# Optimization experiments

Hardware: AMD Instinct MI355X
Metric: run time of the kernel (lower is better)

Reference implementation:

```python
import jax, jax.numpy as jnp
import numpy as np

MAX_K = 4
KAPPA_MAX = 80.0
TEMP = 0.7

NPOINT1, NSAMPLE1 = 128, 32
NPOINT2, NSAMPLE2 = 32, 32


def _sqdist(a, b):
    # a: (B,M,3), b: (B,N,3) -> (B,M,N) squared euclidean distance
    return (jnp.sum(a * a, -1)[:, :, None] + jnp.sum(b * b, -1)[:, None, :]
            - 2.0 * jnp.einsum('bmc,bnc->bmn', a, b))


def _fps(xyz, npoint):
    # farthest point sampling, sequential over npoint (inherent recurrence)
    B, N, _ = xyz.shape
    def step(carry, _):
        dist, far = carry
        centroid = jnp.take_along_axis(xyz, far[:, None, None], axis=1)  # (B,1,3)
        d = jnp.sum((xyz - centroid) ** 2, -1)                            # (B,N)
        dist = jnp.minimum(dist, d)
        nxt = jnp.argmax(dist, -1).astype(jnp.int32)
        return (dist, nxt), far
    init = (jnp.full((B, N), 1e10, xyz.dtype), jnp.zeros((B,), jnp.int32))
    _, idx = jax.lax.scan(step, init, None, length=npoint)
    return jnp.transpose(idx)  # (B, npoint)


def _gather(x, idx):
    # x: (B,N,C), idx: (B,...) int -> (B,...,C)
    return jax.vmap(lambda xb, ib: xb[ib])(x, idx)


def _sa(xyz, feats, npoint, nsample, params, group_all=False):
    # PointNet++ set abstraction: FPS + kNN grouping + shared MLP + max-pool
    if group_all:
        new_xyz = jnp.zeros((xyz.shape[0], 1, 3), xyz.dtype)
        g = xyz[:, None]                                   # (B,1,N,3)
        if feats is not None:
            g = jnp.concatenate([g, feats[:, None]], -1)   # (B,1,N,3+C)
    else:
        fidx = _fps(xyz, npoint)                           # (B,S)
        new_xyz = _gather(xyz, fidx)                       # (B,S,3)
        d = _sqdist(new_xyz, xyz)                          # (B,S,N)
        _, nidx = jax.lax.top_k(-d, nsample)               # (B,S,K) nearest
        g = _gather(xyz, nidx) - new_xyz[:, :, None]       # relative coords
        if feats is not None:
            g = jnp.concatenate([g, _gather(feats, nidx)], -1)
    for w, b in params:                                    # shared 1x1 MLP
        g = jax.nn.relu(g @ w + b)
    return new_xyz, jnp.max(g, axis=2)                     # max over group


def _ln(x, g, b, eps=1e-5):
    m = jnp.mean(x, -1, keepdims=True)
    v = jnp.var(x, -1, keepdims=True)
    return (x - m) * jax.lax.rsqrt(v + eps) * g + b


def setup_inputs() -> dict:
    key = jax.random.key(0)
    ks = iter(jax.random.split(key, 64))
    def p(shape, s=0.05):
        return jax.random.normal(next(ks), shape, jnp.float32) * s
    d = {"xyz": jax.random.normal(next(ks), (32, 16384, 3), jnp.float32)}
    sa_dims = {"sa1": [3, 64, 64, 128], "sa2": [131, 128, 128, 256], "sa3": [259, 256, 512, 1024]}
    for name, dims in sa_dims.items():
        for i in range(3):
            d[f"{name}_w{i}"] = p((dims[i], dims[i + 1]))
            d[f"{name}_b{i}"] = jnp.zeros((dims[i + 1],), jnp.float32)
    d["fc1_w"] = p((1024, 512)); d["fc1_b"] = jnp.zeros((512,), jnp.float32)
    d["ln1_g"] = jnp.ones((512,), jnp.float32); d["ln1_b"] = jnp.zeros((512,), jnp.float32)
    d["fc2_w"] = p((512, 256)); d["fc2_b"] = jnp.zeros((256,), jnp.float32)
    d["ln2_g"] = jnp.ones((256,), jnp.float32); d["ln2_b"] = jnp.zeros((256,), jnp.float32)
    d["pi_w"] = p((256, MAX_K)); d["pi_b"] = jnp.zeros((MAX_K,), jnp.float32)
    d["mu_w"] = p((256, MAX_K * 2)); d["mu_b"] = jnp.zeros((MAX_K * 2,), jnp.float32)
    d["kappa_w"] = p((256, MAX_K)); d["kappa_b"] = jnp.zeros((MAX_K,), jnp.float32)
    return d


def reference(xyz,
              sa1_w0, sa1_b0, sa1_w1, sa1_b1, sa1_w2, sa1_b2,
              sa2_w0, sa2_b0, sa2_w1, sa2_b1, sa2_w2, sa2_b2,
              sa3_w0, sa3_b0, sa3_w1, sa3_b1, sa3_w2, sa3_b2,
              fc1_w, fc1_b, ln1_g, ln1_b, fc2_w, fc2_b, ln2_g, ln2_b,
              pi_w, pi_b, mu_w, mu_b, kappa_w, kappa_b):
    l1x, l1f = _sa(xyz, None, NPOINT1, NSAMPLE1,
                   [(sa1_w0, sa1_b0), (sa1_w1, sa1_b1), (sa1_w2, sa1_b2)])
    l2x, l2f = _sa(l1x, l1f, NPOINT2, NSAMPLE2,
                   [(sa2_w0, sa2_b0), (sa2_w1, sa2_b1), (sa2_w2, sa2_b2)])
    _, l3f = _sa(l2x, l2f, None, None,
                 [(sa3_w0, sa3_b0), (sa3_w1, sa3_b1), (sa3_w2, sa3_b2)], group_all=True)
    x = l3f.reshape(l3f.shape[0], -1)  # (B,1024)
    x = jax.nn.relu(_ln(x @ fc1_w + fc1_b, ln1_g, ln1_b))  # dropout is identity in eval
    x = jax.nn.relu(_ln(x @ fc2_w + fc2_b, ln2_g, ln2_b))
    weight = jax.nn.softmax((x @ pi_w + pi_b) / TEMP, axis=-1)
    mu_raw = (x @ mu_w + mu_b).reshape(-1, MAX_K, 2)
    nrm = jnp.linalg.norm(mu_raw, axis=-1, keepdims=True)
    mu_unit = mu_raw / jnp.maximum(nrm, 1e-4)              # F.normalize(eps=1e-4)
    c, s = mu_unit[..., 0], mu_unit[..., 1]
    n2 = jnp.sqrt(c * c + s * s)
    mask = n2 < 1e-3
    c = jnp.where(mask, 1.0, c)
    s = jnp.where(mask, 0.0, s)
    mu = jnp.arctan2(s, c)
    kappa = jnp.minimum(jax.nn.softplus(x @ kappa_w + kappa_b) + 1e-6, KAPPA_MAX)
    return mu, kappa, weight
```

## Files before the change

kernel.cpp:

```cpp
#include <hip/hip_runtime.h>
#include <math.h>

#define B 32
#define N1 16384
#define NP1 128
#define NS1 32
#define NP2 32
#define NS2 32

#define OFF_L1X   0
#define OFF_G1    12288
#define OFF_L1F   405504
#define OFF_L2X   929792
#define OFF_NIDX2 932864
#define OFF_L2F   965632
#define OFF_L3F   1227776

__global__ __launch_bounds__(1024) void k_fps1(const float* __restrict__ xyz,
                                               float* __restrict__ l1x) {
  const int b = blockIdx.x, t = threadIdx.x;
  const float* xb = xyz + (size_t)b * N1 * 3;
  float px[16], py[16], pz[16], dd[16];
#pragma unroll
  for (int j = 0; j < 16; ++j) {
    int idx = t + (j << 10);
    px[j] = xb[idx * 3 + 0]; py[j] = xb[idx * 3 + 1]; pz[j] = xb[idx * 3 + 2];
    dd[j] = 1e10f;
  }
  __shared__ float swv[16]; __shared__ int swi[16];
  __shared__ float s_cx, s_cy, s_cz; __shared__ int s_far;
  if (t == 0) { s_cx = xb[0]; s_cy = xb[1]; s_cz = xb[2]; }
  __syncthreads();
  for (int it = 0; it < NP1; ++it) {
    float cx = s_cx, cy = s_cy, cz = s_cz;
    if (t == 0) {
      float* o = l1x + ((size_t)b * NP1 + it) * 3;
      o[0] = cx; o[1] = cy; o[2] = cz;
    }
    float bd = -1.f; int bi = 0x7fffffff;
#pragma unroll
    for (int j = 0; j < 16; ++j) {
      float dx = px[j] - cx, dy = py[j] - cy, dz = pz[j] - cz;
      float d = dx * dx + dy * dy + dz * dz;
      float nd = fminf(dd[j], d);
      dd[j] = nd;
      if (nd > bd) { bd = nd; bi = t + (j << 10); }
    }
#pragma unroll
    for (int off = 32; off > 0; off >>= 1) {
      float od = __shfl_down(bd, off);
      int oi = __shfl_down(bi, off);
      if (od > bd || (od == bd && oi < bi)) { bd = od; bi = oi; }
    }
    if ((t & 63) == 0) { swv[t >> 6] = bd; swi[t >> 6] = bi; }
    __syncthreads();
    if (t < 64) {
      if (t < 16) { bd = swv[t]; bi = swi[t]; } else { bd = -1.f; bi = 0x7fffffff; }
#pragma unroll
      for (int off = 8; off > 0; off >>= 1) {
        float od = __shfl_down(bd, off);
        int oi = __shfl_down(bi, off);
        if (od > bd || (od == bd && oi < bi)) { bd = od; bi = oi; }
      }
      if (t == 0) s_far = bi;
    }
    __syncthreads();
    int far = s_far;
    if (t == (far & 1023)) {
      int jw = far >> 10;
#pragma unroll
      for (int j = 0; j < 16; ++j)
        if (j == jw) { s_cx = px[j]; s_cy = py[j]; s_cz = pz[j]; }
    }
    __syncthreads();
  }
}

__device__ __forceinline__ float dist3(const float* __restrict__ xb, int idx,
                                       float cx, float cy, float cz,
                                       float& x, float& y, float& z) {
  x = xb[idx * 3 + 0]; y = xb[idx * 3 + 1]; z = xb[idx * 3 + 2];
  float dx = x - cx, dy = y - cy, dz = z - cz;
  return dx * dx + dy * dy + dz * dz;
}

#define KNN_CAP 512
#define NBIN 2048

__global__ __launch_bounds__(256) void k_knn1(const float* __restrict__ xyz,
                                              const float* __restrict__ l1x,
                                              float* __restrict__ g1) {
  const int t = threadIdx.x;
  const int b = blockIdx.x & 31;
  const int m = blockIdx.x >> 5;
  const float* xb = xyz + (size_t)b * N1 * 3;
  const float* cp = l1x + ((size_t)b * NP1 + m) * 3;
  const float cx = cp[0], cy = cp[1], cz = cp[2];

  __shared__ int hist[NBIN];
  __shared__ float cd[KNN_CAP]; __shared__ int ci[KNN_CAP];
  __shared__ float cpx[KNN_CAP], cpy[KNN_CAP], cpz[KNN_CAP];
  __shared__ int s_cnt, s_cut;
  __shared__ int wsum[4];

  for (int i = t; i < NBIN; i += 256) hist[i] = 0;
  if (t == 0) { s_cnt = 0; s_cut = NBIN - 1; }
  __syncthreads();

  for (int j = 0; j < 64; ++j) {
    float x, y, z;
    float d = dist3(xb, t + (j << 8), cx, cy, cz, x, y, z);
    atomicAdd(&hist[__float_as_uint(d) >> 20], 1);
  }
  __syncthreads();

  {
    int loc = 0;
#pragma unroll
    for (int j = 0; j < 8; ++j) loc += hist[t * 8 + j];
    int v = loc;
#pragma unroll
    for (int off = 1; off < 64; off <<= 1) {
      int u = __shfl_up(v, off);
      if ((t & 63) >= off) v += u;
    }
    if ((t & 63) == 63) wsum[t >> 6] = v;
    __syncthreads();
    int woff = 0;
    for (int w = 0; w < (t >> 6); ++w) woff += wsum[w];
    int incl = v + woff, excl = incl - loc;
    if (excl < NS1 && incl >= NS1) {
      int c = excl;
#pragma unroll
      for (int j = 0; j < 8; ++j) {
        c += hist[t * 8 + j];
        if (c >= NS1) { s_cut = t * 8 + j; break; }
      }
    }
  }
  __syncthreads();
  const unsigned cut = (unsigned)s_cut + 1u;

  for (int j = 0; j < 64; ++j) {
    float x, y, z;
    float d = dist3(xb, t + (j << 8), cx, cy, cz, x, y, z);
    if ((__float_as_uint(d) >> 20) <= cut) {
      int p = atomicAdd(&s_cnt, 1);
      if (p < KNN_CAP) { cd[p] = d; ci[p] = t + (j << 8); cpx[p] = x; cpy[p] = y; cpz[p] = z; }
    }
  }
  __syncthreads();
  const int cnt = (s_cnt < KNN_CAP) ? s_cnt : KNN_CAP;

  float* gout = g1 + ((size_t)(b * NP1 + m)) * NS1 * 3;
  for (int p = t; p < cnt; p += 256) {
    const float dp = cd[p]; const int ip = ci[p];
    int rank = 0;
    for (int q = 0; q < cnt; ++q) {
      float dq = cd[q];
      rank += (dq < dp || (dq == dp && ci[q] < ip)) ? 1 : 0;
    }
    if (rank < NS1) {
      gout[rank * 3 + 0] = cpx[p] - cx;
      gout[rank * 3 + 1] = cpy[p] - cy;
      gout[rank * 3 + 2] = cpz[p] - cz;
    }
  }
}

template <int K, int C, int TPT>
__device__ __forceinline__ void sa_layer(const float* __restrict__ W,
                                         const float* __restrict__ bias,
                                         const float* __restrict__ hin, int instride,
                                         float* __restrict__ hout,
                                         unsigned* __restrict__ om,
                                         float* __restrict__ wst, int t) {
  constexpr int CT = C / 4;
  constexpr int NT = 8 * CT;
  float acc[TPT][4][4];
  int s4[TPT], c4[TPT]; bool on[TPT];
#pragma unroll
  for (int p = 0; p < TPT; ++p) {
    int tile = t + p * 256;
    on[p] = tile < NT;
    int tl = on[p] ? tile : 0;
    s4[p] = (tl / CT) * 4; c4[p] = (tl % CT) * 4;
    float4 bb = *(const float4*)(bias + c4[p]);
#pragma unroll
    for (int i = 0; i < 4; ++i) {
      acc[p][i][0] = bb.x; acc[p][i][1] = bb.y; acc[p][i][2] = bb.z; acc[p][i][3] = bb.w;
    }
  }
  for (int k0 = 0; k0 < K; k0 += 16) {
    const int kc = (K - k0 < 16) ? (K - k0) : 16;
    __syncthreads();
    for (int i = t; i < kc * C; i += 256) wst[i] = W[k0 * C + i];
    __syncthreads();
    if (kc == 16) {
#pragma unroll
      for (int kk = 0; kk < 16; ++kk) {
#pragma unroll
        for (int p = 0; p < TPT; ++p) {
          float4 w = *(const float4*)(wst + kk * C + c4[p]);
#pragma unroll
          for (int i = 0; i < 4; ++i) {
            float a = hin[(s4[p] + i) * instride + (k0 + kk)];
            acc[p][i][0] += a * w.x; acc[p][i][1] += a * w.y;
            acc[p][i][2] += a * w.z; acc[p][i][3] += a * w.w;
          }
        }
      }
    } else {
      for (int kk = 0; kk < kc; ++kk) {
#pragma unroll
        for (int p = 0; p < TPT; ++p) {
          float4 w = *(const float4*)(wst + kk * C + c4[p]);
#pragma unroll
          for (int i = 0; i < 4; ++i) {
            float a = hin[(s4[p] + i) * instride + (k0 + kk)];
            acc[p][i][0] += a * w.x; acc[p][i][1] += a * w.y;
            acc[p][i][2] += a * w.z; acc[p][i][3] += a * w.w;
          }
        }
      }
    }
  }
#pragma unroll
  for (int p = 0; p < TPT; ++p) {
    if (!on[p]) continue;
    if (om) {
#pragma unroll
      for (int j = 0; j < 4; ++j) {
        float vm = fmaxf(fmaxf(fmaxf(acc[p][0][j], acc[p][1][j]),
                               fmaxf(acc[p][2][j], acc[p][3][j])), 0.f);
        atomicMax(&om[c4[p] + j], __float_as_uint(vm));
      }
    } else {
#pragma unroll
      for (int i = 0; i < 4; ++i)
#pragma unroll
        for (int j = 0; j < 4; ++j)
          hout[(s4[p] + i) * C + c4[p] + j] = fmaxf(acc[p][i][j], 0.f);
    }
  }
}

__global__ __launch_bounds__(256) void k_mlp1(const float* __restrict__ g1,
    const float* __restrict__ w0, const float* __restrict__ b0,
    const float* __restrict__ w1, const float* __restrict__ b1,
    const float* __restrict__ w2, const float* __restrict__ b2,
    float* __restrict__ l1f) {
  const int t = threadIdx.x;
  const int b = blockIdx.x & 31, m = blockIdx.x >> 5;
  __shared__ __align__(16) float h0[32 * 4];
  __shared__ __align__(16) float h1[32 * 64];
  __shared__ __align__(16) float h2[32 * 64];
  __shared__ __align__(16) float wst[16 * 128];
  __shared__ unsigned om[128];
  const float* gi = g1 + ((size_t)(b * NP1 + m)) * NS1 * 3;
  if (t < 96) h0[(t / 3) * 4 + (t % 3)] = gi[t];
  if (t < 128) om[t] = 0u;
  __syncthreads();
  sa_layer<3, 64, 1>(w0, b0, h0, 4, h1, nullptr, wst, t);
  sa_layer<64, 64, 1>(w1, b1, h1, 64, h2, nullptr, wst, t);
  sa_layer<64, 128, 1>(w2, b2, h2, 64, nullptr, om, wst, t);
  __syncthreads();
  if (t < 128) l1f[((size_t)(b * NP1 + m)) * 128 + t] = __uint_as_float(om[t]);
}

__global__ __launch_bounds__(128) void k_fps2(const float* __restrict__ l1x,
                                              float* __restrict__ l2x) {
  const int b = blockIdx.x, t = threadIdx.x;
  const float* xb = l1x + (size_t)b * NP1 * 3;
  float px = xb[t * 3], py = xb[t * 3 + 1], pz = xb[t * 3 + 2];
  float dd = 1e10f;
  __shared__ float swv[2]; __shared__ int swi[2];
  __shared__ float s_cx, s_cy, s_cz; __shared__ int s_far;
  if (t == 0) { s_cx = xb[0]; s_cy = xb[1]; s_cz = xb[2]; }
  __syncthreads();
  for (int it = 0; it < NP2; ++it) {
    float cx = s_cx, cy = s_cy, cz = s_cz;
    if (t == 0) {
      float* o = l2x + ((size_t)b * NP2 + it) * 3;
      o[0] = cx; o[1] = cy; o[2] = cz;
    }
    float dx = px - cx, dy = py - cy, dz = pz - cz;
    dd = fminf(dd, dx * dx + dy * dy + dz * dz);
    float bd = dd; int bi = t;
#pragma unroll
    for (int off = 32; off > 0; off >>= 1) {
      float od = __shfl_down(bd, off); int oi = __shfl_down(bi, off);
      if (od > bd || (od == bd && oi < bi)) { bd = od; bi = oi; }
    }
    if ((t & 63) == 0) { swv[t >> 6] = bd; swi[t >> 6] = bi; }
    __syncthreads();
    if (t == 0) {
      if (swv[1] > bd || (swv[1] == bd && swi[1] < bi)) bi = swi[1];
      s_far = bi;
    }
    __syncthreads();
    if (t == s_far) { s_cx = px; s_cy = py; s_cz = pz; }
    __syncthreads();
  }
}

__global__ __launch_bounds__(256) void k_knn2(const float* __restrict__ l1x,
                                              const float* __restrict__ l2x,
                                              int* __restrict__ nidx2) {
  const int b = blockIdx.x, t = threadIdx.x;
  const int lane = t & 63, wv = t >> 6;
  __shared__ float pxs[128], pys[128], pzs[128];
  if (t < 128) {
    pxs[t] = l1x[((size_t)b * NP1 + t) * 3 + 0];
    pys[t] = l1x[((size_t)b * NP1 + t) * 3 + 1];
    pzs[t] = l1x[((size_t)b * NP1 + t) * 3 + 2];
  }
  __syncthreads();
  for (int mc = wv; mc < NP2; mc += 4) {
    const float* cp = l2x + ((size_t)b * NP2 + mc) * 3;
    float cx = cp[0], cy = cp[1], cz = cp[2];
    float dx = pxs[lane] - cx, dy = pys[lane] - cy, dz = pzs[lane] - cz;
    float d0 = dx * dx + dy * dy + dz * dz;
    dx = pxs[lane + 64] - cx; dy = pys[lane + 64] - cy; dz = pzs[lane + 64] - cz;
    float d1 = dx * dx + dy * dy + dz * dz;
    int* no = nidx2 + ((size_t)b * NP2 + mc) * NS2;
    for (int it = 0; it < NS2; ++it) {
      float bv; int bi;
      if (d1 < d0) { bv = d1; bi = lane + 64; } else { bv = d0; bi = lane; }
#pragma unroll
      for (int off = 32; off > 0; off >>= 1) {
        float ov = __shfl_down(bv, off); int oi = __shfl_down(bi, off);
        if (ov < bv || (ov == bv && oi < bi)) { bv = ov; bi = oi; }
      }
      bi = __shfl(bi, 0);
      if (lane == (bi & 63)) { if (bi < 64) d0 = 1e30f; else d1 = 1e30f; }
      if (lane == 0) no[it] = bi;
    }
  }
}

__global__ __launch_bounds__(256) void k_mlp2(const float* __restrict__ l1x,
    const float* __restrict__ l2x, const float* __restrict__ l1f,
    const int* __restrict__ nidx2,
    const float* __restrict__ w0, const float* __restrict__ b0,
    const float* __restrict__ w1, const float* __restrict__ b1,
    const float* __restrict__ w2, const float* __restrict__ b2,
    float* __restrict__ l2f) {
  const int t = threadIdx.x;
  const int b = blockIdx.x & 31, mc = blockIdx.x >> 5;
  __shared__ __align__(16) float h0[32 * 132];
  __shared__ __align__(16) float h1[32 * 128];
  __shared__ __align__(16) float wst[16 * 256];
  __shared__ unsigned om[256];
  __shared__ int sni[32];
  if (t < 32) sni[t] = nidx2[((size_t)b * NP2 + mc) * NS2 + t];
  om[t] = 0u;
  __syncthreads();
  const float* l1fb = l1f + (size_t)b * NP1 * 128;
  for (int i = t; i < 32 * 128; i += 256) {
    int r = i >> 7, cc = i & 127;
    h0[r * 132 + 3 + cc] = l1fb[(size_t)sni[r] * 128 + cc];
  }
  if (t < 96) {
    int r = t / 3, ax = t - 3 * r;
    h0[r * 132 + ax] = l1x[((size_t)b * NP1 + sni[r]) * 3 + ax] -
                       l2x[((size_t)b * NP2 + mc) * 3 + ax];
  }
  __syncthreads();
  sa_layer<131, 128, 1>(w0, b0, h0, 132, h1, nullptr, wst, t);
  sa_layer<128, 128, 1>(w1, b1, h1, 128, h0, nullptr, wst, t);
  sa_layer<128, 256, 2>(w2, b2, h0, 128, nullptr, om, wst, t);
  __syncthreads();
  l2f[((size_t)(b * NP2 + mc)) * 256 + t] = __uint_as_float(om[t]);
}

__global__ __launch_bounds__(512) void k_mlp3(const float* __restrict__ l2x,
    const float* __restrict__ l2f,
    const float* __restrict__ w0, const float* __restrict__ b0,
    const float* __restrict__ w1, const float* __restrict__ b1,
    const float* __restrict__ w2, const float* __restrict__ b2,
    float* __restrict__ l3f) {
  const int t = threadIdx.x;
  const int b = blockIdx.x & 31, sg = blockIdx.x >> 5;
  __shared__ float in[4][260];
  __shared__ float h1[4][256];
  __shared__ float h2[4][512];
  for (int i = t; i < 4 * 256; i += 512) {
    int s = i >> 8, c = i & 255;
    in[s][3 + c] = l2f[((size_t)(b * NP2) + sg * 4 + s) * 256 + c];
  }
  if (t < 12) {
    int s = t / 3, ax = t - 3 * s;
    in[s][ax] = l2x[((size_t)b * NP2 + sg * 4 + s) * 3 + ax];
  }
  __syncthreads();
  if (t < 256) {
    float a0 = b0[t], a1 = a0, a2 = a0, a3 = a0;
    for (int k = 0; k < 259; ++k) {
      float w = w0[k * 256 + t];
      a0 += in[0][k] * w; a1 += in[1][k] * w; a2 += in[2][k] * w; a3 += in[3][k] * w;
    }
    h1[0][t] = fmaxf(a0, 0.f); h1[1][t] = fmaxf(a1, 0.f);
    h1[2][t] = fmaxf(a2, 0.f); h1[3][t] = fmaxf(a3, 0.f);
  }
  __syncthreads();
  {
    float a0 = b1[t], a1 = a0, a2 = a0, a3 = a0;
    for (int k = 0; k < 256; ++k) {
      float w = w1[k * 512 + t];
      a0 += h1[0][k] * w; a1 += h1[1][k] * w; a2 += h1[2][k] * w; a3 += h1[3][k] * w;
    }
    h2[0][t] = fmaxf(a0, 0.f); h2[1][t] = fmaxf(a1, 0.f);
    h2[2][t] = fmaxf(a2, 0.f); h2[3][t] = fmaxf(a3, 0.f);
  }
  __syncthreads();
  {
    float a[2][4];
#pragma unroll
    for (int p = 0; p < 2; ++p) {
      float bv = b2[t + p * 512];
      a[p][0] = bv; a[p][1] = bv; a[p][2] = bv; a[p][3] = bv;
    }
    for (int k = 0; k < 512; ++k) {
      float x0 = h2[0][k], x1 = h2[1][k], x2 = h2[2][k], x3 = h2[3][k];
      float wA = w2[k * 1024 + t];
      float wB = w2[k * 1024 + t + 512];
      a[0][0] += x0 * wA; a[0][1] += x1 * wA; a[0][2] += x2 * wA; a[0][3] += x3 * wA;
      a[1][0] += x0 * wB; a[1][1] += x1 * wB; a[1][2] += x2 * wB; a[1][3] += x3 * wB;
    }
#pragma unroll
    for (int p = 0; p < 2; ++p) {
      float vm = fmaxf(fmaxf(fmaxf(a[p][0], a[p][1]), fmaxf(a[p][2], a[p][3])), 0.f);
      atomicMax((unsigned*)l3f + (size_t)b * 1024 + t + p * 512, __float_as_uint(vm));
    }
  }
}

__global__ __launch_bounds__(256) void k_head(const float* __restrict__ l3f,
    const float* __restrict__ fc1w, const float* __restrict__ fc1b,
    const float* __restrict__ lg1, const float* __restrict__ lb1,
    const float* __restrict__ fc2w, const float* __restrict__ fc2b,
    const float* __restrict__ lg2, const float* __restrict__ lb2,
    const float* __restrict__ piw, const float* __restrict__ pib,
    const float* __restrict__ muw, const float* __restrict__ mub,
    const float* __restrict__ kw, const float* __restrict__ kb,
    float* __restrict__ out) {
  const int b = blockIdx.x, t = threadIdx.x;
  __shared__ float x[1024], x1[512], x2[256];
  __shared__ float red[8];
  __shared__ float hv[16];
  for (int i = t; i < 1024; i += 256) x[i] = l3f[(size_t)b * 1024 + i];
  __syncthreads();
  float a0 = fc1b[t], a1 = fc1b[t + 256];
  for (int k = 0; k < 1024; ++k) {
    float xv = x[k];
    a0 += xv * fc1w[k * 512 + t];
    a1 += xv * fc1w[k * 512 + t + 256];
  }
  {
    float s = a0 + a1, ss = a0 * a0 + a1 * a1;
#pragma unroll
    for (int off = 32; off > 0; off >>= 1) { s += __shfl_down(s, off); ss += __shfl_down(ss, off); }
    if ((t & 63) == 0) { red[t >> 6] = s; red[4 + (t >> 6)] = ss; }
    __syncthreads();
    if (t == 0) {
      float S = red[0] + red[1] + red[2] + red[3];
      float SS = red[4] + red[5] + red[6] + red[7];
      float mean = S / 512.f;
      red[0] = mean; red[4] = SS / 512.f - mean * mean;
    }
    __syncthreads();
    float mean = red[0], var = red[4];
    float rs = rsqrtf(var + 1e-5f);
    x1[t]       = fmaxf((a0 - mean) * rs * lg1[t] + lb1[t], 0.f);
    x1[t + 256] = fmaxf((a1 - mean) * rs * lg1[t + 256] + lb1[t + 256], 0.f);
  }
  __syncthreads();
  float a = fc2b[t];
  for (int k = 0; k < 512; ++k) a += x1[k] * fc2w[k * 256 + t];
  {
    float s = a, ss = a * a;
#pragma unroll
    for (int off = 32; off > 0; off >>= 1) { s += __shfl_down(s, off); ss += __shfl_down(ss, off); }
    if ((t & 63) == 0) { red[t >> 6] = s; red[4 + (t >> 6)] = ss; }
    __syncthreads();
    if (t == 0) {
      float S = red[0] + red[1] + red[2] + red[3];
      float SS = red[4] + red[5] + red[6] + red[7];
      float mean = S / 256.f;
      red[0] = mean; red[4] = SS / 256.f - mean * mean;
    }
    __syncthreads();
    float mean = red[0], var = red[4];
    x2[t] = fmaxf((a - mean) * rsqrtf(var + 1e-5f) * lg2[t] + lb2[t], 0.f);
  }
  __syncthreads();
  if (t < 16) {
    const float* W; const float* bb; int c; int C;
    if (t < 4)        { W = piw; bb = pib; c = t;      C = 4; }
    else if (t < 12)  { W = muw; bb = mub; c = t - 4;  C = 8; }
    else              { W = kw;  bb = kb;  c = t - 12; C = 4; }
    float acc = bb[c];
    for (int k = 0; k < 256; ++k) acc += x2[k] * W[k * C + c];
    hv[t] = acc;
  }
  __syncthreads();
  if (t == 0) {
    float z[4], mx = -1e30f;
#pragma unroll
    for (int i = 0; i < 4; ++i) { z[i] = hv[i] / 0.7f; mx = fmaxf(mx, z[i]); }
    float e[4], sum = 0.f;
#pragma unroll
    for (int i = 0; i < 4; ++i) { e[i] = expf(z[i] - mx); sum += e[i]; }
#pragma unroll
    for (int k = 0; k < 4; ++k) {
      float c0 = hv[4 + 2 * k], s0 = hv[4 + 2 * k + 1];
      float nr = sqrtf(c0 * c0 + s0 * s0);
      float den = fmaxf(nr, 1e-4f);
      float cu = c0 / den, su = s0 / den;
      float n2 = sqrtf(cu * cu + su * su);
      if (n2 < 1e-3f) { cu = 1.f; su = 0.f; }
      out[b * 4 + k] = atan2f(su, cu);
      float zk = hv[12 + k];
      float sp = fmaxf(zk, 0.f) + log1pf(expf(-fabsf(zk)));
      out[128 + b * 4 + k] = fminf(sp + 1e-6f, 80.f);
      out[256 + b * 4 + k] = e[k] / sum;
    }
  }
}

extern "C" void kernel_launch(void* const* d_in, const int* in_sizes, int n_in,
                              void* d_out, int out_size, void* d_ws, size_t ws_size,
                              hipStream_t stream) {
  const float* xyz  = (const float*)d_in[0];
  const float* s1w0 = (const float*)d_in[1];  const float* s1b0 = (const float*)d_in[2];
  const float* s1w1 = (const float*)d_in[3];  const float* s1b1 = (const float*)d_in[4];
  const float* s1w2 = (const float*)d_in[5];  const float* s1b2 = (const float*)d_in[6];
  const float* s2w0 = (const float*)d_in[7];  const float* s2b0 = (const float*)d_in[8];
  const float* s2w1 = (const float*)d_in[9];  const float* s2b1 = (const float*)d_in[10];
  const float* s2w2 = (const float*)d_in[11]; const float* s2b2 = (const float*)d_in[12];
  const float* s3w0 = (const float*)d_in[13]; const float* s3b0 = (const float*)d_in[14];
  const float* s3w1 = (const float*)d_in[15]; const float* s3b1 = (const float*)d_in[16];
  const float* s3w2 = (const float*)d_in[17]; const float* s3b2 = (const float*)d_in[18];
  const float* fc1w = (const float*)d_in[19]; const float* fc1b = (const float*)d_in[20];
  const float* lg1  = (const float*)d_in[21]; const float* lb1  = (const float*)d_in[22];
  const float* fc2w = (const float*)d_in[23]; const float* fc2b = (const float*)d_in[24];
  const float* lg2  = (const float*)d_in[25]; const float* lb2  = (const float*)d_in[26];
  const float* piw  = (const float*)d_in[27]; const float* pib  = (const float*)d_in[28];
  const float* muw  = (const float*)d_in[29]; const float* mub  = (const float*)d_in[30];
  const float* kw   = (const float*)d_in[31]; const float* kb   = (const float*)d_in[32];

  float* ws   = (float*)d_ws;
  float* l1x  = ws + OFF_L1X;
  float* g1   = ws + OFF_G1;
  float* l1f  = ws + OFF_L1F;
  float* l2x  = ws + OFF_L2X;
  int*   nid2 = (int*)(ws + OFF_NIDX2);
  float* l2f  = ws + OFF_L2F;
  float* l3f  = ws + OFF_L3F;
  float* out  = (float*)d_out;

  hipMemsetAsync(l3f, 0, (size_t)B * 1024 * sizeof(float), stream);
  k_fps1<<<B, 1024, 0, stream>>>(xyz, l1x);
  k_knn1<<<B * NP1, 256, 0, stream>>>(xyz, l1x, g1);
  k_mlp1<<<B * NP1, 256, 0, stream>>>(g1, s1w0, s1b0, s1w1, s1b1, s1w2, s1b2, l1f);
  k_fps2<<<B, 128, 0, stream>>>(l1x, l2x);
  k_knn2<<<B, 256, 0, stream>>>(l1x, l2x, nid2);
  k_mlp2<<<B * NP2, 256, 0, stream>>>(l1x, l2x, l1f, nid2,
                                      s2w0, s2b0, s2w1, s2b1, s2w2, s2b2, l2f);
  k_mlp3<<<B * 8, 512, 0, stream>>>(l2x, l2f, s3w0, s3b0, s3w1, s3b1, s3w2, s3b2, l3f);
  k_head<<<B, 256, 0, stream>>>(l3f, fc1w, fc1b, lg1, lb1, fc2w, fc2b, lg2, lb2,
                                piw, pib, muw, mub, kw, kb, out);
}
```

Before: 1.010 ms.

## Replace FPS block reduction with packed 64-bit key shared atomicMax

Each iteration of farthest-point sampling now packs distance and inverted index into one 64-bit key, reduces it within each wavefront with a single shuffle chain, and merges wavefronts through a shared-memory atomicMax into a double-buffered slot. This drops the second-stage wave reduction and one of the barriers, and the next centroid is read from global memory by index instead of being broadcast by the owning thread. Because distances are non-negative, their float bits order correctly as unsigned integers, and inverting the index keeps the lowest-index tie-break. The trade-offs are 64-bit shuffles, a shared 64-bit atomic per wave, and a dependent global load of the centroid on the serial per-iteration path.

```diff
diff --git a/kernel.cpp b/kernel.cpp
--- a/kernel.cpp
+++ b/kernel.cpp
@@ -27,51 +27,39 @@
     px[j] = xb[idx * 3 + 0]; py[j] = xb[idx * 3 + 1]; pz[j] = xb[idx * 3 + 2];
     dd[j] = 1e10f;
   }
-  __shared__ float swv[16]; __shared__ int swi[16];
-  __shared__ float s_cx, s_cy, s_cz; __shared__ int s_far;
-  if (t == 0) { s_cx = xb[0]; s_cy = xb[1]; s_cz = xb[2]; }
+  __shared__ unsigned long long slot[2];
+  if (t == 0) { slot[0] = 0xFFFFFFFFull; slot[1] = 0ull; }
   __syncthreads();
   for (int it = 0; it < NP1; ++it) {
-    float cx = s_cx, cy = s_cy, cz = s_cz;
+    const unsigned long long key = slot[it & 1];
+    const int widx = (int)(0xFFFFFFFFu - (unsigned)(key & 0xFFFFFFFFull));
+    const float cx = xb[widx * 3 + 0];
+    const float cy = xb[widx * 3 + 1];
+    const float cz = xb[widx * 3 + 2];
     if (t == 0) {
       float* o = l1x + ((size_t)b * NP1 + it) * 3;
       o[0] = cx; o[1] = cy; o[2] = cz;
     }
-    float bd = -1.f; int bi = 0x7fffffff;
+    __syncthreads();
+    if (t == 0) slot[it & 1] = 0ull;
+    float bd = -1.f; int bj = 0;
 #pragma unroll
     for (int j = 0; j < 16; ++j) {
       float dx = px[j] - cx, dy = py[j] - cy, dz = pz[j] - cz;
       float d = dx * dx + dy * dy + dz * dz;
       float nd = fminf(dd[j], d);
       dd[j] = nd;
-      if (nd > bd) { bd = nd; bi = t + (j << 10); }
-    }
+      if (nd > bd) { bd = nd; bj = j; }
+    }
+    unsigned long long mykey =
+        ((unsigned long long)__float_as_uint(bd) << 32) |
+        (unsigned long long)(0xFFFFFFFFu - (unsigned)(t + (bj << 10)));
 #pragma unroll
     for (int off = 32; off > 0; off >>= 1) {
-      float od = __shfl_down(bd, off);
-      int oi = __shfl_down(bi, off);
-      if (od > bd || (od == bd && oi < bi)) { bd = od; bi = oi; }
-    }
-    if ((t & 63) == 0) { swv[t >> 6] = bd; swi[t >> 6] = bi; }
-    __syncthreads();
-    if (t < 64) {
-      if (t < 16) { bd = swv[t]; bi = swi[t]; } else { bd = -1.f; bi = 0x7fffffff; }
-#pragma unroll
-      for (int off = 8; off > 0; off >>= 1) {
-        float od = __shfl_down(bd, off);
-        int oi = __shfl_down(bi, off);
-        if (od > bd || (od == bd && oi < bi)) { bd = od; bi = oi; }
-      }
-      if (t == 0) s_far = bi;
-    }
-    __syncthreads();
-    int far = s_far;
-    if (t == (far & 1023)) {
-      int jw = far >> 10;
-#pragma unroll
-      for (int j = 0; j < 16; ++j)
-        if (j == jw) { s_cx = px[j]; s_cy = py[j]; s_cz = pz[j]; }
-    }
+      unsigned long long ok = __shfl_down(mykey, off);
+      if (ok > mykey) mykey = ok;
+    }
+    if ((t & 63) == 0) atomicMax(&slot[(it + 1) & 1], mykey);
     __syncthreads();
   }
 }
```

Result: faster. 940.8 us (-6.8%).
